# Performance work log

Measured on AMD Instinct MI355X. Metric: run time of the kernel, lower is better.

The kernel has to match this reference:

```python
import jax, jax.numpy as jnp
import numpy as np

B, C, H, W = 32, 64, 128, 128

def setup_inputs() -> dict:
    key = jax.random.key(0)
    k1, k2, k3, k4 = jax.random.split(key, 4)
    x = jax.random.normal(k1, (B, C, H, W), dtype=jnp.float32)
    theta = jax.random.normal(k2, (C, C), dtype=jnp.float32) * (6.0 / (C + C)) ** 0.5  # xavier-ish
    W_lin = jax.random.normal(k3, (C, C), dtype=jnp.float32) * (1.0 / C) ** 0.5
    b_lin = jax.random.normal(k4, (C,), dtype=jnp.float32) * 0.01
    return {"x": x, "theta": theta, "W_lin": W_lin, "b_lin": b_lin}

def reference(x, theta, W_lin, b_lin):
    b, c, h, w = x.shape
    # channel descriptor: global average pool -> [B, C]
    wvec = jnp.mean(x, axis=(2, 3))
    # pairwise diff and soft adjacency, batched over B
    diff = wvec[:, :, None] - wvec[:, None, :]              # [B, C, C]
    e = jnp.exp(-diff)
    T = jnp.abs(1.0 - e / (1.0 + e)) - 1.0                  # [B, C, C]
    A = 0.5 * (T + jnp.swapaxes(T, 1, 2)) * theta           # [B, C, C]
    # graph conv: A @ x_flat, relu
    x_flat = x.reshape(b, c, h * w)                         # [B, C, HW]
    Hmat = jax.nn.relu(jnp.einsum('bij,bjn->bin', A, x_flat))  # [B, C, HW]
    # Linear over channel dim applied to H.T: [B, HW, C]
    Hout = jnp.einsum('bin,ci->bnc', Hmat, W_lin) + b_lin   # [B, HW, C]
    # faithful to torch: H.view(C, h, w) is a raw row-major reshape of [HW, C]
    return Hout.reshape(b, c, h, w)
```

## Files before the change

### kernel.cpp

```cpp
#include <hip/hip_runtime.h>

static constexpr int Cc  = 64;
static constexpr int HWc = 16384;
static constexpr int Bc  = 32;
static constexpr int NT  = 256;


typedef _Float16 v8h __attribute__((ext_vector_type(8)));
typedef float    v4f __attribute__((ext_vector_type(4)));

union FragU { uint32_t u[4]; v8h h; };

__device__ inline uint32_t packf2(float lo, float hi) {
  union { _Float16 h[2]; uint32_t u; } r;
  r.h[0] = (_Float16)lo; r.h[1] = (_Float16)hi;
  return r.u;
}

__global__ void prep_weights(const float* __restrict__ theta,
                             const float* __restrict__ Wlin,
                             _Float16* __restrict__ M1h,
                             _Float16* __restrict__ Wh) {
  int t = blockIdx.x * 256 + threadIdx.x;
  if (t < Cc * Cc) {
    M1h[t] = (_Float16)(-0.5f * theta[t]);
    Wh[t]  = (_Float16)(Wlin[t]);
  }
}

__global__ __launch_bounds__(256) void fused_mfma(
    const float* __restrict__ x,
    const _Float16* __restrict__ M1h,
    const _Float16* __restrict__ Wh,
    const float* __restrict__ blin,
    float* __restrict__ out)
{
  __shared__ __align__(16) union {
    uint32_t xp[32][260];
    _Float16 p2[4][64][72];
  } lds;

  const int tid = threadIdx.x;
  const int b   = blockIdx.x >> 6;
  const int n0  = (blockIdx.x & 63) * NT;

  const float* xb = x + (size_t)b * Cc * HWc + n0;
#pragma unroll
  for (int rep = 0; rep < 8; ++rep) {
    const int chunk = rep * 256 + tid;
    const int p   = chunk >> 6;
    const int col = (chunk & 63) * 4;
    const float4 e = *(const float4*)(xb + (size_t)(2 * p)     * HWc + col);
    const float4 o = *(const float4*)(xb + (size_t)(2 * p + 1) * HWc + col);
    uint4 w;
    w.x = packf2(e.x, o.x); w.y = packf2(e.y, o.y);
    w.z = packf2(e.z, o.z); w.w = packf2(e.w, o.w);
    *(uint4*)&lds.xp[p][col] = w;
  }
  __syncthreads();

  const int wv   = tid >> 6;
  const int lq   = tid & 15;
  const int quad = (tid & 63) >> 4;
  const int nw   = wv * 64;

  FragU a1[4][2];
#pragma unroll
  for (int mt = 0; mt < 4; ++mt)
#pragma unroll
    for (int kt = 0; kt < 2; ++kt)
#pragma unroll
      for (int r = 0; r < 4; ++r)
        a1[mt][kt].u[r] = lds.xp[kt * 16 + quad * 4 + r][nw + mt * 16 + lq];

  const v8h* M1v = (const v8h*)M1h;
  v8h b1[4][2];
#pragma unroll
  for (int it = 0; it < 4; ++it)
#pragma unroll
    for (int kt = 0; kt < 2; ++kt)
      b1[it][kt] = M1v[(it * 16 + lq) * 8 + kt * 4 + quad];

  v4f acc1[4][4];
#pragma unroll
  for (int mt = 0; mt < 4; ++mt)
#pragma unroll
    for (int it = 0; it < 4; ++it) {
      v4f a = {0.f, 0.f, 0.f, 0.f};
#pragma unroll
      for (int kt = 0; kt < 2; ++kt)
        a = __builtin_amdgcn_mfma_f32_16x16x32_f16(a1[mt][kt].h, b1[it][kt], a, 0, 0, 0);
      acc1[mt][it] = a;
    }

  __syncthreads();

#pragma unroll
  for (int mt = 0; mt < 4; ++mt)
#pragma unroll
    for (int it = 0; it < 4; ++it)
#pragma unroll
      for (int r = 0; r < 4; ++r)
        lds.p2[wv][mt * 16 + quad * 4 + r][it * 16 + lq] =
            (_Float16)fmaxf(acc1[mt][it][r], 0.f);
  __syncthreads();

  const v8h* Whv = (const v8h*)Wh;
  v8h b2[4][2];
#pragma unroll
  for (int ct = 0; ct < 4; ++ct)
#pragma unroll
    for (int kt = 0; kt < 2; ++kt)
      b2[ct][kt] = Whv[(ct * 16 + lq) * 8 + kt * 4 + quad];

  float bias[4];
#pragma unroll
  for (int ct = 0; ct < 4; ++ct) bias[ct] = blin[ct * 16 + lq];

  const size_t outbase = ((size_t)b * HWc + n0 + nw) * Cc;
#pragma unroll
  for (int mt = 0; mt < 4; ++mt) {
    FragU a2[2];
#pragma unroll
    for (int kt = 0; kt < 2; ++kt)
      a2[kt].h = *(const v8h*)&lds.p2[wv][mt * 16 + lq][kt * 32 + quad * 8];
#pragma unroll
    for (int ct = 0; ct < 4; ++ct) {
      v4f a = {bias[ct], bias[ct], bias[ct], bias[ct]};
#pragma unroll
      for (int kt = 0; kt < 2; ++kt)
        a = __builtin_amdgcn_mfma_f32_16x16x32_f16(a2[kt].h, b2[ct][kt], a, 0, 0, 0);
#pragma unroll
      for (int r = 0; r < 4; ++r)
        out[outbase + (size_t)(mt * 16 + quad * 4 + r) * Cc + ct * 16 + lq] = a[r];
    }
  }
}

extern "C" void kernel_launch(void* const* d_in, const int* in_sizes, int n_in,
                              void* d_out, int out_size, void* d_ws, size_t ws_size,
                              hipStream_t stream) {
  const float* x     = (const float*)d_in[0];
  const float* theta = (const float*)d_in[1];
  const float* W_lin = (const float*)d_in[2];
  const float* b_lin = (const float*)d_in[3];
  float* out = (float*)d_out;

  _Float16* M1h = (_Float16*)d_ws;
  _Float16* Wh  = M1h + Cc * Cc;

  prep_weights<<<(Cc * Cc + 255) / 256, 256, 0, stream>>>(theta, W_lin, M1h, Wh);

  const int nblocks = Bc * HWc / NT;
  fused_mfma<<<nblocks, 256, 0, stream>>>(x, M1h, Wh, b_lin, out);
}
```

Measured before the change: 240.3 us.

## Make fused MFMA kernel persistent over tiles with double-buffered prefetch

Each block now handles four 128-column tiles instead of one 256-column tile. It double-buffers the packed fp16 input in LDS and prefetches the next tile's global loads into registers while the current tile's MFMAs run. The operand order of the MFMAs is swapped so each lane holds four consecutive output channels, which turns the output stores into vector float4 writes, and the two weight fragments and bias are loaded once per block. The goal is to hide global load latency and cut the number of store instructions. In exchange the kernel uses more registers and LDS (launch bounds min 3 blocks) and runs fewer blocks.

```diff
diff --git a/kernel.cpp b/kernel.cpp
--- a/kernel.cpp
+++ b/kernel.cpp
@@ -3,7 +3,8 @@
 static constexpr int Cc  = 64;
 static constexpr int HWc = 16384;
 static constexpr int Bc  = 32;
-static constexpr int NT  = 256;
+static constexpr int NT  = 128;
+static constexpr int TPB = 4;
 
 
 typedef _Float16 v8h __attribute__((ext_vector_type(8)));
@@ -17,6 +18,10 @@
   return r.u;
 }
 
+__device__ inline v4f mfma16(v8h a, v8h b, v4f c) {
+  return __builtin_amdgcn_mfma_f32_16x16x32_f16(a, b, c, 0, 0, 0);
+}
+
 __global__ void prep_weights(const float* __restrict__ theta,
                              const float* __restrict__ Wlin,
                              _Float16* __restrict__ M1h,
@@ -28,111 +33,129 @@
   }
 }
 
-__global__ __launch_bounds__(256) void fused_mfma(
+__global__ __launch_bounds__(256, 3) void fused_mfma(
     const float* __restrict__ x,
     const _Float16* __restrict__ M1h,
     const _Float16* __restrict__ Wh,
     const float* __restrict__ blin,
     float* __restrict__ out)
 {
-  __shared__ __align__(16) union {
-    uint32_t xp[32][260];
-    _Float16 p2[4][64][72];
-  } lds;
+  __shared__ __align__(16) uint32_t  xp[2][32][132];
+  __shared__ __align__(16) _Float16  p2[4][32][72];
 
-  const int tid = threadIdx.x;
-  const int b   = blockIdx.x >> 6;
-  const int n0  = (blockIdx.x & 63) * NT;
-
-  const float* xb = x + (size_t)b * Cc * HWc + n0;
-#pragma unroll
-  for (int rep = 0; rep < 8; ++rep) {
-    const int chunk = rep * 256 + tid;
-    const int p   = chunk >> 6;
-    const int col = (chunk & 63) * 4;
-    const float4 e = *(const float4*)(xb + (size_t)(2 * p)     * HWc + col);
-    const float4 o = *(const float4*)(xb + (size_t)(2 * p + 1) * HWc + col);
-    uint4 w;
-    w.x = packf2(e.x, o.x); w.y = packf2(e.y, o.y);
-    w.z = packf2(e.z, o.z); w.w = packf2(e.w, o.w);
-    *(uint4*)&lds.xp[p][col] = w;
-  }
-  __syncthreads();
+  const int tid   = threadIdx.x;
+  const int tile0 = blockIdx.x * TPB;
+  const int b     = tile0 >> 7;
+  const int n00   = (tile0 & 127) * NT;
+  const float* xb = x + (size_t)b * Cc * HWc;
 
   const int wv   = tid >> 6;
   const int lq   = tid & 15;
   const int quad = (tid & 63) >> 4;
-  const int nw   = wv * 64;
+  const int nw   = wv * 32;
 
-  FragU a1[4][2];
+  const int sp   = tid >> 5;
+  const int scol = (tid & 31) * 4;
+
+  {
+    const float* xt = xb + n00;
 #pragma unroll
-  for (int mt = 0; mt < 4; ++mt)
-#pragma unroll
-    for (int kt = 0; kt < 2; ++kt)
-#pragma unroll
-      for (int r = 0; r < 4; ++r)
-        a1[mt][kt].u[r] = lds.xp[kt * 16 + quad * 4 + r][nw + mt * 16 + lq];
+    for (int rep = 0; rep < 4; ++rep) {
+      const int p = rep * 8 + sp;
+      const float4 e = *(const float4*)(xt + (size_t)(2 * p)     * HWc + scol);
+      const float4 o = *(const float4*)(xt + (size_t)(2 * p + 1) * HWc + scol);
+      uint4 w;
+      w.x = packf2(e.x, o.x); w.y = packf2(e.y, o.y);
+      w.z = packf2(e.z, o.z); w.w = packf2(e.w, o.w);
+      *(uint4*)&xp[0][p][scol] = w;
+    }
+  }
 
   const v8h* M1v = (const v8h*)M1h;
-  v8h b1[4][2];
+  const v8h* Whv = (const v8h*)Wh;
+  v8h w1[4][2], w2[4][2];
 #pragma unroll
   for (int it = 0; it < 4; ++it)
 #pragma unroll
-    for (int kt = 0; kt < 2; ++kt)
-      b1[it][kt] = M1v[(it * 16 + lq) * 8 + kt * 4 + quad];
-
-  v4f acc1[4][4];
+    for (int kt = 0; kt < 2; ++kt) {
+      w1[it][kt] = M1v[(it * 16 + lq) * 8 + kt * 4 + quad];
+      w2[it][kt] = Whv[(it * 16 + lq) * 8 + kt * 4 + quad];
+    }
+  v4f bias4[4];
 #pragma unroll
-  for (int mt = 0; mt < 4; ++mt)
-#pragma unroll
-    for (int it = 0; it < 4; ++it) {
-      v4f a = {0.f, 0.f, 0.f, 0.f};
-#pragma unroll
-      for (int kt = 0; kt < 2; ++kt)
-        a = __builtin_amdgcn_mfma_f32_16x16x32_f16(a1[mt][kt].h, b1[it][kt], a, 0, 0, 0);
-      acc1[mt][it] = a;
-    }
+  for (int ct = 0; ct < 4; ++ct)
+    bias4[ct] = *(const v4f*)(blin + ct * 16 + quad * 4);
 
   __syncthreads();
 
 #pragma unroll
-  for (int mt = 0; mt < 4; ++mt)
+  for (int t = 0; t < TPB; ++t) {
+    const int cur = t & 1;
+
+    float4 pf[8];
+    if (t < TPB - 1) {
+      const float* xt = xb + n00 + (t + 1) * NT;
+#pragma unroll
+      for (int rep = 0; rep < 4; ++rep) {
+        const int p = rep * 8 + sp;
+        pf[2 * rep]     = *(const float4*)(xt + (size_t)(2 * p)     * HWc + scol);
+        pf[2 * rep + 1] = *(const float4*)(xt + (size_t)(2 * p + 1) * HWc + scol);
+      }
+    }
+
+    FragU xf[2][2];
+#pragma unroll
+    for (int nt = 0; nt < 2; ++nt)
+#pragma unroll
+      for (int kt = 0; kt < 2; ++kt)
+#pragma unroll
+        for (int r = 0; r < 4; ++r)
+          xf[nt][kt].u[r] = xp[cur][kt * 16 + quad * 4 + r][nw + nt * 16 + lq];
+
 #pragma unroll
     for (int it = 0; it < 4; ++it)
 #pragma unroll
-      for (int r = 0; r < 4; ++r)
-        lds.p2[wv][mt * 16 + quad * 4 + r][it * 16 + lq] =
-            (_Float16)fmaxf(acc1[mt][it][r], 0.f);
-  __syncthreads();
+      for (int nt = 0; nt < 2; ++nt) {
+        v4f a = {0.f, 0.f, 0.f, 0.f};
+#pragma unroll
+        for (int kt = 0; kt < 2; ++kt)
+          a = mfma16(w1[it][kt], xf[nt][kt].h, a);
+        uint2 w;
+        w.x = packf2(fmaxf(a[0], 0.f), fmaxf(a[1], 0.f));
+        w.y = packf2(fmaxf(a[2], 0.f), fmaxf(a[3], 0.f));
+        *(uint2*)&p2[wv][nt * 16 + lq][it * 16 + quad * 4] = w;
+      }
 
-  const v8h* Whv = (const v8h*)Wh;
-  v8h b2[4][2];
+    const size_t orow0 = ((size_t)b * HWc + n00 + t * NT + nw) * Cc;
 #pragma unroll
-  for (int ct = 0; ct < 4; ++ct)
-#pragma unroll
-    for (int kt = 0; kt < 2; ++kt)
-      b2[ct][kt] = Whv[(ct * 16 + lq) * 8 + kt * 4 + quad];
-
-  float bias[4];
-#pragma unroll
-  for (int ct = 0; ct < 4; ++ct) bias[ct] = blin[ct * 16 + lq];
-
-  const size_t outbase = ((size_t)b * HWc + n0 + nw) * Cc;
-#pragma unroll
-  for (int mt = 0; mt < 4; ++mt) {
-    FragU a2[2];
-#pragma unroll
-    for (int kt = 0; kt < 2; ++kt)
-      a2[kt].h = *(const v8h*)&lds.p2[wv][mt * 16 + lq][kt * 32 + quad * 8];
-#pragma unroll
-    for (int ct = 0; ct < 4; ++ct) {
-      v4f a = {bias[ct], bias[ct], bias[ct], bias[ct]};
+    for (int nt = 0; nt < 2; ++nt) {
+      FragU pr[2];
 #pragma unroll
       for (int kt = 0; kt < 2; ++kt)
-        a = __builtin_amdgcn_mfma_f32_16x16x32_f16(a2[kt].h, b2[ct][kt], a, 0, 0, 0);
+        pr[kt].h = *(const v8h*)&p2[wv][nt * 16 + lq][kt * 32 + quad * 8];
+      float* orow = out + orow0 + (size_t)(nt * 16 + lq) * Cc + quad * 4;
 #pragma unroll
-      for (int r = 0; r < 4; ++r)
-        out[outbase + (size_t)(mt * 16 + quad * 4 + r) * Cc + ct * 16 + lq] = a[r];
+      for (int ct = 0; ct < 4; ++ct) {
+        v4f a = bias4[ct];
+#pragma unroll
+        for (int kt = 0; kt < 2; ++kt)
+          a = mfma16(w2[ct][kt], pr[kt].h, a);
+        *(v4f*)(orow + ct * 16) = a;
+      }
+    }
+
+    if (t < TPB - 1) {
+#pragma unroll
+      for (int rep = 0; rep < 4; ++rep) {
+        const int p = rep * 8 + sp;
+        uint4 w;
+        w.x = packf2(pf[2 * rep].x, pf[2 * rep + 1].x);
+        w.y = packf2(pf[2 * rep].y, pf[2 * rep + 1].y);
+        w.z = packf2(pf[2 * rep].z, pf[2 * rep + 1].z);
+        w.w = packf2(pf[2 * rep].w, pf[2 * rep + 1].w);
+        *(uint4*)&xp[cur ^ 1][p][scol] = w;
+      }
+      __syncthreads();
     }
   }
 }
@@ -151,6 +174,6 @@
 
   prep_weights<<<(Cc * Cc + 255) / 256, 256, 0, stream>>>(theta, W_lin, M1h, Wh);
 
-  const int nblocks = Bc * HWc / NT;
+  const int nblocks = Bc * HWc / (NT * TPB);
   fused_mfma<<<nblocks, 256, 0, stream>>>(x, M1h, Wh, b_lin, out);
 }
```

After: 246.4 us. 1.03x slower.
